# Kernel tuning notes

Measured on AMD Instinct MI355X. Metric: run time of the kernel, lower is better.

The kernel has to match this reference:

```python
import jax, jax.numpy as jnp
import numpy as np

N, M, DIM, OUT_DIM = 50000, 512, 256, 256
NEG = -1e9


def setup_inputs() -> dict:
    key = jax.random.key(0)
    k1, k2, k3, k4, k5, k6 = jax.random.split(key, 6)
    node_features = jax.random.normal(k1, (N, DIM), dtype=jnp.float32)
    # each node assigned to one molecule (sorted segment ids)
    mol_ids = jnp.sort(jax.random.randint(k2, (N,), 0, M))
    mol_node_matrix = (mol_ids[None, :] == jnp.arange(M)[:, None]).astype(jnp.float32)  # [M, N]
    mol_node_mask = jnp.where(mol_node_matrix > 0, 0.0, NEG).astype(jnp.float32)  # [M, N]
    # Linear params (PyTorch-style uniform init)
    bound = 1.0 / np.sqrt(DIM)
    W_attend = jax.random.uniform(k3, (DIM, OUT_DIM), minval=-bound, maxval=bound, dtype=jnp.float32)
    b_attend = jax.random.uniform(k4, (OUT_DIM,), minval=-bound, maxval=bound, dtype=jnp.float32)
    w_align = jax.random.uniform(k5, (DIM, 1), minval=-bound, maxval=bound, dtype=jnp.float32)
    b_align = jax.random.uniform(k6, (1,), minval=-bound, maxval=bound, dtype=jnp.float32)
    return {"node_features": node_features, "mol_node_matrix": mol_node_matrix,
            "mol_node_mask": mol_node_mask, "W_attend": W_attend, "b_attend": b_attend,
            "w_align": w_align, "b_align": b_align}


def reference(node_features, mol_node_matrix, mol_node_mask, W_attend, b_attend, w_align, b_align):
    # h = LeakyReLU(attend(x)) : [N, out_dim]
    h = jax.nn.leaky_relu(node_features @ W_attend + b_attend, negative_slope=0.01)
    # a = align(x) : [N]  (dropout p=0 -> identity)
    a = (node_features @ w_align + b_align)[:, 0]
    # mol_node_matrix @ diag(a) == mol_node_matrix * a[None, :]  (same math, no NxN diag)
    logits = mol_node_matrix * a[None, :] + mol_node_mask  # [M, N]
    mol_node_weight = jax.nn.softmax(logits, axis=1)
    return mol_node_weight @ h, mol_node_weight
```

## Files before the change

### kernel.cpp

```cpp
#include <hip/hip_runtime.h>
#include <cstdint>
#include <cstddef>

#define N_NODES 50000
#define M_MOLS  512
#define DIMK    256
#define ODIM    256

#define NCH   99
#define CW    32
#define NSAMP (NCH * CW)
#define NGAP  (NCH - 1)

#define NB_SAMP  NCH
#define NB_ALIGN 1563
#define NB_WPACK 32
#define P1_GRID  (NB_SAMP + NB_ALIGN + NB_WPACK)

#define POOL_BLOCKS 512
#define WCHUNK 49
#define WROWS  8
#define NB_WEIGHT (WCHUNK * (M_MOLS / WROWS))
#define C_GRID (POOL_BLOCKS + NB_WEIGHT)

typedef float  f32x4  __attribute__((ext_vector_type(4)));
typedef __bf16 bf16x8 __attribute__((ext_vector_type(8)));

static __device__ __forceinline__ short f2bf(float f) {
  unsigned u = __builtin_bit_cast(unsigned, f);
  u = u + 0x7fffu + ((u >> 16) & 1u);
  return (short)(u >> 16);
}

static __device__ __forceinline__ int chunk_base(int c) {
  return (c < NCH - 1) ? c * 512 : (N_NODES - CW);
}

__global__ __launch_bounds__(256) void k_phase1(
    const float* __restrict__ x, const float* __restrict__ mat,
    const float* __restrict__ W, const float* __restrict__ wa,
    const float* __restrict__ ba,
    float* __restrict__ a, int* __restrict__ smolid, int4* __restrict__ wp) {
  int b = blockIdx.x, t = threadIdx.x;
  if (b < NB_SAMP) {
    int base = chunk_base(b);
    int cp = (t & 15) * 2;
    int rg = t >> 4;
    int idx = -1, idy = -1;
    const float* p0 = mat + (size_t)(rg * 32) * N_NODES + base + cp;
#pragma unroll 16
    for (int r = 0; r < 32; r++) {
      float2 v = *(const float2*)(p0 + (size_t)r * N_NODES);
      if (v.x != 0.f) idx = rg * 32 + r;
      if (v.y != 0.f) idy = rg * 32 + r;
    }
    __shared__ int sm[16][32];
    sm[rg][cp] = idx; sm[rg][cp + 1] = idy;
    __syncthreads();
    if (t < 32) {
      int best = -1;
#pragma unroll
      for (int g = 0; g < 16; g++) best = max(best, sm[g][t]);
      smolid[b * CW + t] = best;
    }
  } else if (b < NB_SAMP + NB_ALIGN) {
    int tid = (b - NB_SAMP) * 256 + t;
    int row = tid >> 3, sub = tid & 7;
    if (row >= N_NODES) return;
    const float4* xr = (const float4*)(x + (size_t)row * DIMK) + sub * 8;
    const float4* wr = (const float4*)wa + sub * 8;
    float s = 0.f;
#pragma unroll
    for (int i = 0; i < 8; i++) {
      float4 xv = xr[i], wv = wr[i];
      s += xv.x * wv.x + xv.y * wv.y + xv.z * wv.z + xv.w * wv.w;
    }
    s += __shfl_xor(s, 1); s += __shfl_xor(s, 2); s += __shfl_xor(s, 4);
    if (sub == 0) a[row] = s + ba[0];
  } else {
    int g  = (b - NB_SAMP - NB_ALIGN) * 256 + t;
    int l  = g & 63;
    int Ju = g >> 6;
    int J  = Ju >> 3, u = Ju & 7;
    int j  = J * 16 + (l & 15);
    int k0 = u * 32 + (l >> 4) * 8;
    short sv[8];
#pragma unroll
    for (int i = 0; i < 8; i++) sv[i] = f2bf(W[(size_t)(k0 + i) * ODIM + j]);
    wp[Ju * 64 + l] = *(int4*)sv;
  }
}

__global__ __launch_bounds__(256) void k_bounds(
    const float* __restrict__ mat, const int* __restrict__ smolid,
    int* __restrict__ strt) {
  int b = blockIdx.x, t = threadIdx.x;
  if (b < NGAP) {
    int p  = chunk_base(b) + CW - 1;
    int q  = chunk_base(b + 1);
    int ag = smolid[b * CW + CW - 1];
    int bg = smolid[(b + 1) * CW];
    if (bg == ag) return;
    int Wd = q - p;
    int nr = bg - ag;
    __shared__ int f1[512];
    int wave = t >> 6, l = t & 63;
    for (int rr = wave; rr < nr; rr += 4) {
      const float* rp = mat + (size_t)(ag + 1 + rr) * N_NODES + p + 1;
      int mn = 0x7fffffff;
      for (int i = l; i < Wd; i += 64)
        if (rp[i] != 0.f) { mn = i; break; }
#pragma unroll
      for (int o = 1; o < 64; o <<= 1) mn = min(mn, __shfl_xor(mn, o));
      if (l == 0) f1[rr] = mn;
    }
    __syncthreads();
    if (t == 0) {
      int run = 0x7fffffff;
      for (int rr = nr - 1; rr >= 0; rr--) {
        run = min(run, f1[rr]);
        strt[ag + 1 + rr] = p + 1 + run;
      }
    }
  } else if (b < NGAP + NCH) {
    int cc = b - NGAP;
    if (t >= 1 && t < CW) {
      int prev = smolid[cc * CW + t - 1], cur = smolid[cc * CW + t];
      int col = chunk_base(cc) + t;
      for (int m = prev + 1; m <= cur; m++) strt[m] = col;
    }
  } else {
    int first = smolid[0], last = smolid[NSAMP - 1];
    for (int m = t; m <= M_MOLS; m += 256) {
      if (m <= first) strt[m] = 0;
      else if (m > last) strt[m] = N_NODES;
    }
  }
}

__global__ __launch_bounds__(256) void k_stats(
    const float* __restrict__ a, const int* __restrict__ strt,
    float* __restrict__ wval) {
  int m = blockIdx.x, t = threadIdx.x;
  int s = strt[m], e = strt[m + 1];

  float mx = -3e38f;
  for (int i = s + t; i < e; i += 256) mx = fmaxf(mx, a[i]);
#pragma unroll
  for (int o = 1; o < 64; o <<= 1) mx = fmaxf(mx, __shfl_xor(mx, o));
  __shared__ float r0[4];
  if ((t & 63) == 0) r0[t >> 6] = mx;
  __syncthreads();
  mx = fmaxf(fmaxf(r0[0], r0[1]), fmaxf(r0[2], r0[3]));

  float sm = 0.f;
  for (int i = s + t; i < e; i += 256) sm += __expf(a[i] - mx);
#pragma unroll
  for (int o = 1; o < 64; o <<= 1) sm += __shfl_xor(sm, o);
  __shared__ float r1[4];
  if ((t & 63) == 0) r1[t >> 6] = sm;
  __syncthreads();
  sm = r1[0] + r1[1] + r1[2] + r1[3];
  float inv = (sm > 0.f) ? 1.f / sm : 0.f;

  for (int i = s + t; i < e; i += 256) wval[i] = __expf(a[i] - mx) * inv;
}

__global__ __launch_bounds__(256, 2) void k_phase3(
    const float* __restrict__ x, const float* __restrict__ wval,
    const int* __restrict__ strt, const int4* __restrict__ wp,
    const float* __restrict__ bias, float* __restrict__ out0,
    float* __restrict__ out1) {
  int b  = blockIdx.x;
  int pb = b / 7;
  bool isPool = ((b % 7) == 0) && (pb < POOL_BLOCKS);

  if (!isPool) {
    int before = (pb < POOL_BLOCKS) ? (pb + 1) : POOL_BLOCKS;
    int wb = b - before;
    int mc = wb / WCHUNK;
    int c  = wb % WCHUNK;
    int t  = threadIdx.x;
    int n4 = c * 256 + t;
    if (n4 >= N_NODES / 4) return;
    int n = n4 * 4;
    float4 w = *(const float4*)(wval + n);
    int m0 = mc * WROWS;
#pragma unroll
    for (int r = 0; r < WROWS; r++) {
      int m = m0 + r;
      int s = strt[m], e = strt[m + 1];
      float4 o;
      o.x = ((unsigned)(n     - s) < (unsigned)(e - s)) ? w.x : 0.f;
      o.y = ((unsigned)(n + 1 - s) < (unsigned)(e - s)) ? w.y : 0.f;
      o.z = ((unsigned)(n + 2 - s) < (unsigned)(e - s)) ? w.z : 0.f;
      o.w = ((unsigned)(n + 3 - s) < (unsigned)(e - s)) ? w.w : 0.f;
      *(float4*)(out1 + (size_t)m * N_NODES + n) = o;
    }
    return;
  }

  int m = pb;
  int s = strt[m], e = strt[m + 1];
  int tid  = threadIdx.x;
  int wave = tid >> 6, l = tid & 63;

  bf16x8 wfrag[4][8];
#pragma unroll
  for (int t2 = 0; t2 < 4; t2++)
#pragma unroll
    for (int u = 0; u < 8; u++) {
      int Ju = (wave * 4 + t2) * 8 + u;
      wfrag[t2][u] = __builtin_bit_cast(bf16x8, wp[Ju * 64 + l]);
    }
  float bias_r[4];
#pragma unroll
  for (int t2 = 0; t2 < 4; t2++) bias_r[t2] = bias[wave * 64 + t2 * 16 + (l & 15)];

  float pooled[4] = {0.f, 0.f, 0.f, 0.f};

  __shared__ __align__(16) short xs[16 * 256];
  __shared__ float wt[16];

  int r = l & 15, g = l >> 4;
  int swr = (r & 7) << 4;

  int nt = (e - s + 15) >> 4;
  for (int tile = 0; tile < nt; ++tile) {
    int base = s + tile * 16;
    __syncthreads();
    {
      int row = tid >> 4;
      int c0  = (tid & 15) * 16;
      int n   = base + row;
      float v[16];
      if (n < e) {
        const float4* src = (const float4*)(x + (size_t)n * DIMK + c0);
        float4 A = src[0], B = src[1], C = src[2], D = src[3];
        v[0]=A.x; v[1]=A.y; v[2]=A.z; v[3]=A.w;
        v[4]=B.x; v[5]=B.y; v[6]=B.z; v[7]=B.w;
        v[8]=C.x; v[9]=C.y; v[10]=C.z; v[11]=C.w;
        v[12]=D.x; v[13]=D.y; v[14]=D.z; v[15]=D.w;
      } else {
#pragma unroll
        for (int i = 0; i < 16; i++) v[i] = 0.f;
      }
      short sv[16];
#pragma unroll
      for (int i = 0; i < 16; i++) sv[i] = f2bf(v[i]);
      int sw = (row & 7) << 4;
      char* lb = (char*)xs;
      *(int4*)(lb + (row << 9) + (((c0 << 1)     ) ^ sw)) = *(int4*)(sv);
      *(int4*)(lb + (row << 9) + (((c0 << 1) + 16) ^ sw)) = *(int4*)(sv + 8);
      if (tid < 16) {
        int nn = base + tid;
        wt[tid] = (nn < e) ? wval[nn] : 0.f;
      }
    }
    __syncthreads();
    bf16x8 af[8];
    const char* lb = (const char*)xs;
#pragma unroll
    for (int u = 0; u < 8; u++) {
      int addr = (r << 9) + ((((u << 6) + (g << 4))) ^ swr);
      af[u] = __builtin_bit_cast(bf16x8, *(const int4*)(lb + addr));
    }
#pragma unroll
    for (int t2 = 0; t2 < 4; t2++) {
      f32x4 acc = {0.f, 0.f, 0.f, 0.f};
#pragma unroll
      for (int u = 0; u < 8; u++)
        acc = __builtin_amdgcn_mfma_f32_16x16x32_bf16(af[u], wfrag[t2][u], acc, 0, 0, 0);
      float p = 0.f;
#pragma unroll
      for (int i = 0; i < 4; i++) {
        float h = acc[i] + bias_r[t2];
        h = h > 0.f ? h : 0.01f * h;
        p += wt[(g << 2) + i] * h;
      }
      pooled[t2] += p;
    }
  }
#pragma unroll
  for (int t2 = 0; t2 < 4; t2++) {
    float p = pooled[t2];
    p += __shfl_xor(p, 16);
    p += __shfl_xor(p, 32);
    pooled[t2] = p;
  }
  if (l < 16) {
#pragma unroll
    for (int t2 = 0; t2 < 4; t2++)
      out0[m * ODIM + wave * 64 + t2 * 16 + l] = pooled[t2];
  }
}

extern "C" void kernel_launch(void* const* d_in, const int* in_sizes, int n_in,
                              void* d_out, int out_size, void* d_ws, size_t ws_size,
                              hipStream_t stream) {
  const float* x   = (const float*)d_in[0];
  const float* mat = (const float*)d_in[1];
  const float* W   = (const float*)d_in[3];
  const float* bA  = (const float*)d_in[4];
  const float* wa  = (const float*)d_in[5];
  const float* ba  = (const float*)d_in[6];

  float* out0 = (float*)d_out;
  float* out1 = out0 + (size_t)M_MOLS * ODIM;

  char*  ws     = (char*)d_ws;
  float* a      = (float*)(ws);
  int*   smolid = (int*)  (ws + 200064);
  int*   strt   = (int*)  (ws + 212800);
  float* wval   = (float*)(ws + 214912);
  int4*  wp     = (int4*) (ws + 414912);

  k_phase1<<<P1_GRID, 256, 0, stream>>>(x, mat, W, wa, ba, a, smolid, wp);
  k_bounds<<<NGAP + NCH + 1, 256, 0, stream>>>(mat, smolid, strt);
  k_stats <<<M_MOLS, 256, 0, stream>>>(a, strt, wval);
  k_phase3<<<C_GRID, 256, 0, stream>>>(x, wval, strt, wp, bA, out0, out1);
}
```

Baseline: 59.28 us.

## Fuse bounds, align, softmax, weight write and pooling into one per-molecule kernel

Collapses four launches into two. Each molecule block now finds its own segment bounds by binary search over the sampled ids plus a local mask scan, computes align logits into LDS, does the softmax there, writes its weight row including zeros, and runs the MFMA pooling with 512 threads. This drops the global a/wval/strt round trips and the separate weight-write blocks. The cost is less parallelism: only 512 blocks each write a full 200KB row, segments longer than 4096 nodes would overflow the LDS buffer, and each wave now covers only half of the output columns.

```diff
diff --git a/kernel.cpp b/kernel.cpp
--- a/kernel.cpp
+++ b/kernel.cpp
@@ -10,18 +10,14 @@
 #define NCH   99
 #define CW    32
 #define NSAMP (NCH * CW)
-#define NGAP  (NCH - 1)
 
 #define NB_SAMP  NCH
-#define NB_ALIGN 1563
 #define NB_WPACK 32
-#define P1_GRID  (NB_SAMP + NB_ALIGN + NB_WPACK)
-
-#define POOL_BLOCKS 512
-#define WCHUNK 49
-#define WROWS  8
-#define NB_WEIGHT (WCHUNK * (M_MOLS / WROWS))
-#define C_GRID (POOL_BLOCKS + NB_WEIGHT)
+#define K1_GRID  (NB_SAMP + NB_WPACK)
+
+#define K2T   512
+#define A_CAP 4096
+#define NF4   (N_NODES / 4)
 
 typedef float  f32x4  __attribute__((ext_vector_type(4)));
 typedef __bf16 bf16x8 __attribute__((ext_vector_type(8)));
@@ -35,12 +31,13 @@
 static __device__ __forceinline__ int chunk_base(int c) {
   return (c < NCH - 1) ? c * 512 : (N_NODES - CW);
 }
-
-__global__ __launch_bounds__(256) void k_phase1(
-    const float* __restrict__ x, const float* __restrict__ mat,
-    const float* __restrict__ W, const float* __restrict__ wa,
-    const float* __restrict__ ba,
-    float* __restrict__ a, int* __restrict__ smolid, int4* __restrict__ wp) {
+static __device__ __forceinline__ int scol(int idx) {
+  return chunk_base(idx >> 5) + (idx & 31);
+}
+
+__global__ __launch_bounds__(256) void k_prep(
+    const float* __restrict__ mat, const float* __restrict__ W,
+    int* __restrict__ smolid, int4* __restrict__ wp) {
   int b = blockIdx.x, t = threadIdx.x;
   if (b < NB_SAMP) {
     int base = chunk_base(b);
@@ -63,22 +60,8 @@
       for (int g = 0; g < 16; g++) best = max(best, sm[g][t]);
       smolid[b * CW + t] = best;
     }
-  } else if (b < NB_SAMP + NB_ALIGN) {
-    int tid = (b - NB_SAMP) * 256 + t;
-    int row = tid >> 3, sub = tid & 7;
-    if (row >= N_NODES) return;
-    const float4* xr = (const float4*)(x + (size_t)row * DIMK) + sub * 8;
-    const float4* wr = (const float4*)wa + sub * 8;
-    float s = 0.f;
-#pragma unroll
-    for (int i = 0; i < 8; i++) {
-      float4 xv = xr[i], wv = wr[i];
-      s += xv.x * wv.x + xv.y * wv.y + xv.z * wv.z + xv.w * wv.w;
-    }
-    s += __shfl_xor(s, 1); s += __shfl_xor(s, 2); s += __shfl_xor(s, 4);
-    if (sub == 0) a[row] = s + ba[0];
   } else {
-    int g  = (b - NB_SAMP - NB_ALIGN) * 256 + t;
+    int g  = (b - NB_SAMP) * 256 + t;
     int l  = g & 63;
     int Ju = g >> 6;
     int J  = Ju >> 3, u = Ju & 7;
@@ -91,182 +74,168 @@
   }
 }
 
-__global__ __launch_bounds__(256) void k_bounds(
-    const float* __restrict__ mat, const int* __restrict__ smolid,
-    int* __restrict__ strt) {
-  int b = blockIdx.x, t = threadIdx.x;
-  if (b < NGAP) {
-    int p  = chunk_base(b) + CW - 1;
-    int q  = chunk_base(b + 1);
-    int ag = smolid[b * CW + CW - 1];
-    int bg = smolid[(b + 1) * CW];
-    if (bg == ag) return;
-    int Wd = q - p;
-    int nr = bg - ag;
-    __shared__ int f1[512];
-    int wave = t >> 6, l = t & 63;
-    for (int rr = wave; rr < nr; rr += 4) {
-      const float* rp = mat + (size_t)(ag + 1 + rr) * N_NODES + p + 1;
-      int mn = 0x7fffffff;
-      for (int i = l; i < Wd; i += 64)
-        if (rp[i] != 0.f) { mn = i; break; }
-#pragma unroll
-      for (int o = 1; o < 64; o <<= 1) mn = min(mn, __shfl_xor(mn, o));
-      if (l == 0) f1[rr] = mn;
-    }
-    __syncthreads();
-    if (t == 0) {
-      int run = 0x7fffffff;
-      for (int rr = nr - 1; rr >= 0; rr--) {
-        run = min(run, f1[rr]);
-        strt[ag + 1 + rr] = p + 1 + run;
-      }
-    }
-  } else if (b < NGAP + NCH) {
-    int cc = b - NGAP;
-    if (t >= 1 && t < CW) {
-      int prev = smolid[cc * CW + t - 1], cur = smolid[cc * CW + t];
-      int col = chunk_base(cc) + t;
-      for (int m = prev + 1; m <= cur; m++) strt[m] = col;
-    }
-  } else {
-    int first = smolid[0], last = smolid[NSAMP - 1];
-    for (int m = t; m <= M_MOLS; m += 256) {
-      if (m <= first) strt[m] = 0;
-      else if (m > last) strt[m] = N_NODES;
-    }
-  }
-}
-
-__global__ __launch_bounds__(256) void k_stats(
-    const float* __restrict__ a, const int* __restrict__ strt,
-    float* __restrict__ wval) {
-  int m = blockIdx.x, t = threadIdx.x;
-  int s = strt[m], e = strt[m + 1];
-
-  float mx = -3e38f;
-  for (int i = s + t; i < e; i += 256) mx = fmaxf(mx, a[i]);
-#pragma unroll
-  for (int o = 1; o < 64; o <<= 1) mx = fmaxf(mx, __shfl_xor(mx, o));
-  __shared__ float r0[4];
-  if ((t & 63) == 0) r0[t >> 6] = mx;
-  __syncthreads();
-  mx = fmaxf(fmaxf(r0[0], r0[1]), fmaxf(r0[2], r0[3]));
-
-  float sm = 0.f;
-  for (int i = s + t; i < e; i += 256) sm += __expf(a[i] - mx);
-#pragma unroll
-  for (int o = 1; o < 64; o <<= 1) sm += __shfl_xor(sm, o);
-  __shared__ float r1[4];
-  if ((t & 63) == 0) r1[t >> 6] = sm;
-  __syncthreads();
-  sm = r1[0] + r1[1] + r1[2] + r1[3];
-  float inv = (sm > 0.f) ? 1.f / sm : 0.f;
-
-  for (int i = s + t; i < e; i += 256) wval[i] = __expf(a[i] - mx) * inv;
-}
-
-__global__ __launch_bounds__(256, 2) void k_phase3(
-    const float* __restrict__ x, const float* __restrict__ wval,
-    const int* __restrict__ strt, const int4* __restrict__ wp,
+__global__ __launch_bounds__(K2T, 2) void k_main(
+    const float* __restrict__ x, const float* __restrict__ mat,
+    const float* __restrict__ wa, const float* __restrict__ ba,
+    const int* __restrict__ smolid, const int4* __restrict__ wp,
     const float* __restrict__ bias, float* __restrict__ out0,
     float* __restrict__ out1) {
-  int b  = blockIdx.x;
-  int pb = b / 7;
-  bool isPool = ((b % 7) == 0) && (pb < POOL_BLOCKS);
-
-  if (!isPool) {
-    int before = (pb < POOL_BLOCKS) ? (pb + 1) : POOL_BLOCKS;
-    int wb = b - before;
-    int mc = wb / WCHUNK;
-    int c  = wb % WCHUNK;
-    int t  = threadIdx.x;
-    int n4 = c * 256 + t;
-    if (n4 >= N_NODES / 4) return;
-    int n = n4 * 4;
-    float4 w = *(const float4*)(wval + n);
-    int m0 = mc * WROWS;
-#pragma unroll
-    for (int r = 0; r < WROWS; r++) {
-      int m = m0 + r;
-      int s = strt[m], e = strt[m + 1];
-      float4 o;
-      o.x = ((unsigned)(n     - s) < (unsigned)(e - s)) ? w.x : 0.f;
-      o.y = ((unsigned)(n + 1 - s) < (unsigned)(e - s)) ? w.y : 0.f;
-      o.z = ((unsigned)(n + 2 - s) < (unsigned)(e - s)) ? w.z : 0.f;
-      o.w = ((unsigned)(n + 3 - s) < (unsigned)(e - s)) ? w.w : 0.f;
-      *(float4*)(out1 + (size_t)m * N_NODES + n) = o;
-    }
-    return;
-  }
-
-  int m = pb;
-  int s = strt[m], e = strt[m + 1];
-  int tid  = threadIdx.x;
-  int wave = tid >> 6, l = tid & 63;
-
-  bf16x8 wfrag[4][8];
-#pragma unroll
-  for (int t2 = 0; t2 < 4; t2++)
-#pragma unroll
-    for (int u = 0; u < 8; u++) {
-      int Ju = (wave * 4 + t2) * 8 + u;
-      wfrag[t2][u] = __builtin_bit_cast(bf16x8, wp[Ju * 64 + l]);
-    }
-  float bias_r[4];
-#pragma unroll
-  for (int t2 = 0; t2 < 4; t2++) bias_r[t2] = bias[wave * 64 + t2 * 16 + (l & 15)];
-
-  float pooled[4] = {0.f, 0.f, 0.f, 0.f};
-
+  int m = blockIdx.x;
+  int t = threadIdx.x;
+
+  __shared__ float a_lds[A_CAP];
   __shared__ __align__(16) short xs[16 * 256];
-  __shared__ float wt[16];
-
+  __shared__ float fred[8];
+  __shared__ int   ired[8];
+  __shared__ int   sseg[2];
+
+  for (int which = 0; which < 2; which++) {
+    int mm = m + which;
+    int lo = 0, hi = NSAMP;
+    while (lo < hi) { int mid = (lo + hi) >> 1; if (smolid[mid] < mm) lo = mid + 1; else hi = mid; }
+    int res;
+    if (lo == 0) res = 0;
+    else if (lo >= NSAMP) res = N_NODES;
+    else {
+      int chi = scol(lo), clo = scol(lo - 1);
+      if (chi == clo + 1) res = chi;
+      else {
+        int bh = smolid[lo];
+        res = -1;
+        for (int r = mm; r <= bh; r++) {
+          int f = 0x7fffffff;
+          int col = clo + 1 + t;
+          if (col <= chi && mat[(size_t)r * N_NODES + col] != 0.f) f = col;
+#pragma unroll
+          for (int o = 1; o < 64; o <<= 1) f = min(f, __shfl_xor(f, o));
+          if ((t & 63) == 0) ired[t >> 6] = f;
+          __syncthreads();
+          int gmin = ired[0];
+#pragma unroll
+          for (int i = 1; i < 8; i++) gmin = min(gmin, ired[i]);
+          __syncthreads();
+          if (gmin != 0x7fffffff) { res = gmin; break; }
+        }
+        if (res < 0) res = chi;
+      }
+    }
+    if (t == 0) sseg[which] = res;
+  }
+  __syncthreads();
+  int seg_s = sseg[0], seg_e = sseg[1];
+  int L = seg_e - seg_s;
+
+  int s4 = seg_s >> 2, e4 = (seg_e + 3) >> 2;
+  float4* orow = (float4*)out1 + (size_t)m * NF4;
+  float4 zz; zz.x = zz.y = zz.z = zz.w = 0.f;
+  for (int q = t; q < NF4; q += K2T)
+    if (q < s4 || q >= e4) orow[q] = zz;
+
+  float ba0 = ba[0];
+  int sub = t & 7;
+  float4 wv[8];
+  {
+    const float4* wr = (const float4*)wa + sub * 8;
+#pragma unroll
+    for (int i = 0; i < 8; i++) wv[i] = wr[i];
+  }
+  int nit = (L + 63) >> 6;
+  for (int it = 0; it < nit; it++) {
+    int ro  = it * 64 + (t >> 3);
+    int row = seg_s + ro;
+    float s = 0.f;
+    if (row < seg_e) {
+      const float4* xr = (const float4*)(x + (size_t)row * DIMK) + sub * 8;
+#pragma unroll
+      for (int i = 0; i < 8; i++) {
+        float4 xv = xr[i];
+        s += xv.x * wv[i].x + xv.y * wv[i].y + xv.z * wv[i].z + xv.w * wv[i].w;
+      }
+    }
+    s += __shfl_xor(s, 1); s += __shfl_xor(s, 2); s += __shfl_xor(s, 4);
+    if (sub == 0 && row < seg_e && ro < A_CAP) a_lds[ro] = s + ba0;
+  }
+  __syncthreads();
+
+  float mx = -3e38f;
+  for (int i = t; i < L; i += K2T) mx = fmaxf(mx, a_lds[i]);
+#pragma unroll
+  for (int o = 1; o < 64; o <<= 1) mx = fmaxf(mx, __shfl_xor(mx, o));
+  if ((t & 63) == 0) fred[t >> 6] = mx;
+  __syncthreads();
+  mx = fred[0];
+#pragma unroll
+  for (int i = 1; i < 8; i++) mx = fmaxf(mx, fred[i]);
+  __syncthreads();
+  float sm = 0.f;
+  for (int i = t; i < L; i += K2T) sm += __expf(a_lds[i] - mx);
+#pragma unroll
+  for (int o = 1; o < 64; o <<= 1) sm += __shfl_xor(sm, o);
+  if ((t & 63) == 0) fred[t >> 6] = sm;
+  __syncthreads();
+  sm = 0.f;
+#pragma unroll
+  for (int i = 0; i < 8; i++) sm += fred[i];
+  float inv = (sm > 0.f) ? 1.f / sm : 0.f;
+  for (int i = t; i < L; i += K2T) a_lds[i] = __expf(a_lds[i] - mx) * inv;
+  __syncthreads();
+
+  for (int q = s4 + t; q < e4; q += K2T) {
+    int n = q * 4;
+    float4 o;
+    o.x = (n     >= seg_s && n     < seg_e) ? a_lds[n     - seg_s] : 0.f;
+    o.y = (n + 1 >= seg_s && n + 1 < seg_e) ? a_lds[n + 1 - seg_s] : 0.f;
+    o.z = (n + 2 >= seg_s && n + 2 < seg_e) ? a_lds[n + 2 - seg_s] : 0.f;
+    o.w = (n + 3 >= seg_s && n + 3 < seg_e) ? a_lds[n + 3 - seg_s] : 0.f;
+    orow[q] = o;
+  }
+
+  int wv_id = t >> 6, l = t & 63;
+  bf16x8 wfrag[2][8];
+#pragma unroll
+  for (int t2 = 0; t2 < 2; t2++)
+#pragma unroll
+    for (int u = 0; u < 8; u++)
+      wfrag[t2][u] = __builtin_bit_cast(bf16x8, wp[((wv_id * 2 + t2) * 8 + u) * 64 + l]);
+  float bias_r[2];
+#pragma unroll
+  for (int t2 = 0; t2 < 2; t2++) bias_r[t2] = bias[wv_id * 32 + t2 * 16 + (l & 15)];
+
+  float pooled[2] = {0.f, 0.f};
   int r = l & 15, g = l >> 4;
   int swr = (r & 7) << 4;
 
-  int nt = (e - s + 15) >> 4;
-  for (int tile = 0; tile < nt; ++tile) {
-    int base = s + tile * 16;
+  int srow = t >> 5;
+  int c0b  = (t & 31) * 16;
+  int ssw  = (srow & 7) << 4;
+  char* lb = (char*)xs;
+
+  int nt2 = (L + 15) >> 4;
+  for (int tile = 0; tile < nt2; tile++) {
+    int base = seg_s + tile * 16;
     __syncthreads();
     {
-      int row = tid >> 4;
-      int c0  = (tid & 15) * 16;
-      int n   = base + row;
-      float v[16];
-      if (n < e) {
-        const float4* src = (const float4*)(x + (size_t)n * DIMK + c0);
-        float4 A = src[0], B = src[1], C = src[2], D = src[3];
-        v[0]=A.x; v[1]=A.y; v[2]=A.z; v[3]=A.w;
-        v[4]=B.x; v[5]=B.y; v[6]=B.z; v[7]=B.w;
-        v[8]=C.x; v[9]=C.y; v[10]=C.z; v[11]=C.w;
-        v[12]=D.x; v[13]=D.y; v[14]=D.z; v[15]=D.w;
+      int n = base + srow;
+      short sv[8];
+      if (n < seg_e) {
+        const float4* src = (const float4*)(x + (size_t)n * DIMK) + (t & 31) * 2;
+        float4 A = src[0], B = src[1];
+        sv[0] = f2bf(A.x); sv[1] = f2bf(A.y); sv[2] = f2bf(A.z); sv[3] = f2bf(A.w);
+        sv[4] = f2bf(B.x); sv[5] = f2bf(B.y); sv[6] = f2bf(B.z); sv[7] = f2bf(B.w);
       } else {
 #pragma unroll
-        for (int i = 0; i < 16; i++) v[i] = 0.f;
-      }
-      short sv[16];
-#pragma unroll
-      for (int i = 0; i < 16; i++) sv[i] = f2bf(v[i]);
-      int sw = (row & 7) << 4;
-      char* lb = (char*)xs;
-      *(int4*)(lb + (row << 9) + (((c0 << 1)     ) ^ sw)) = *(int4*)(sv);
-      *(int4*)(lb + (row << 9) + (((c0 << 1) + 16) ^ sw)) = *(int4*)(sv + 8);
-      if (tid < 16) {
-        int nn = base + tid;
-        wt[tid] = (nn < e) ? wval[nn] : 0.f;
-      }
+        for (int i = 0; i < 8; i++) sv[i] = 0;
+      }
+      *(int4*)(lb + (srow << 9) + (c0b ^ ssw)) = *(int4*)sv;
     }
     __syncthreads();
     bf16x8 af[8];
-    const char* lb = (const char*)xs;
-#pragma unroll
-    for (int u = 0; u < 8; u++) {
-      int addr = (r << 9) + ((((u << 6) + (g << 4))) ^ swr);
-      af[u] = __builtin_bit_cast(bf16x8, *(const int4*)(lb + addr));
-    }
-#pragma unroll
-    for (int t2 = 0; t2 < 4; t2++) {
+#pragma unroll
+    for (int u = 0; u < 8; u++)
+      af[u] = __builtin_bit_cast(bf16x8,
+                *(const int4*)(lb + (r << 9) + (((u << 6) + (g << 4)) ^ swr)));
+#pragma unroll
+    for (int t2 = 0; t2 < 2; t2++) {
       f32x4 acc = {0.f, 0.f, 0.f, 0.f};
 #pragma unroll
       for (int u = 0; u < 8; u++)
@@ -274,15 +243,17 @@
       float p = 0.f;
 #pragma unroll
       for (int i = 0; i < 4; i++) {
+        int ridx = tile * 16 + (g << 2) + i;
+        float wgt = (ridx < L) ? a_lds[ridx] : 0.f;
         float h = acc[i] + bias_r[t2];
         h = h > 0.f ? h : 0.01f * h;
-        p += wt[(g << 2) + i] * h;
+        p += wgt * h;
       }
       pooled[t2] += p;
     }
   }
 #pragma unroll
-  for (int t2 = 0; t2 < 4; t2++) {
+  for (int t2 = 0; t2 < 2; t2++) {
     float p = pooled[t2];
     p += __shfl_xor(p, 16);
     p += __shfl_xor(p, 32);
@@ -290,8 +261,8 @@
   }
   if (l < 16) {
 #pragma unroll
-    for (int t2 = 0; t2 < 4; t2++)
-      out0[m * ODIM + wave * 64 + t2 * 16 + l] = pooled[t2];
+    for (int t2 = 0; t2 < 2; t2++)
+      out0[m * ODIM + wv_id * 32 + t2 * 16 + l] = pooled[t2];
   }
 }
 
@@ -308,15 +279,10 @@
   float* out0 = (float*)d_out;
   float* out1 = out0 + (size_t)M_MOLS * ODIM;
 
-  char*  ws     = (char*)d_ws;
-  float* a      = (float*)(ws);
-  int*   smolid = (int*)  (ws + 200064);
-  int*   strt   = (int*)  (ws + 212800);
-  float* wval   = (float*)(ws + 214912);
-  int4*  wp     = (int4*) (ws + 414912);
-
-  k_phase1<<<P1_GRID, 256, 0, stream>>>(x, mat, W, wa, ba, a, smolid, wp);
-  k_bounds<<<NGAP + NCH + 1, 256, 0, stream>>>(mat, smolid, strt);
-  k_stats <<<M_MOLS, 256, 0, stream>>>(a, strt, wval);
-  k_phase3<<<C_GRID, 256, 0, stream>>>(x, wval, strt, wp, bA, out0, out1);
-}
+  char* ws     = (char*)d_ws;
+  int*  smolid = (int*) (ws);
+  int4* wp     = (int4*)(ws + 16384);
+
+  k_prep<<<K1_GRID, 256, 0, stream>>>(mat, W, smolid, wp);
+  k_main<<<M_MOLS, K2T, 0, stream>>>(x, mat, wa, ba, smolid, wp, bA, out0, out1);
+}
```

After: 48.34 us. -18.4%, faster.
